# Performance work log

Hardware: AMD Instinct MI355X
Metric: run time of the kernel (lower is better)

Reference implementation:

```python
import jax, jax.numpy as jnp
import numpy as np

B, T, D, H, STRIDE, MLP = 2, 2048, 1024, 16, 8, 4096
HD = D // H
EPS = 1e-5


def _ln(x, g, b):
    m = x.mean(-1, keepdims=True)
    v = x.var(-1, keepdims=True)
    return (x - m) * jax.lax.rsqrt(v + EPS) * g + b


def setup_inputs() -> dict:
    key = jax.random.key(0)
    ks = jax.random.split(key, 6)
    s = lambda k, shape: (jax.random.normal(k, shape, jnp.float32) * 0.02)
    return {
        "x": jax.random.normal(ks[0], (B, T, D), jnp.float32),
        "w_in": s(ks[1], (3 * D, D)),   # torch in_proj_weight
        "b_in": jnp.zeros((3 * D,), jnp.float32),
        "w_out": s(ks[2], (D, D)),      # attn out_proj
        "b_out": jnp.zeros((D,), jnp.float32),
        "w1": s(ks[3], (MLP, D)),       # mlp first Linear (torch layout [out,in])
        "b1": jnp.zeros((MLP,), jnp.float32),
        "w2": s(ks[4], (D, MLP)),       # mlp second Linear
        "b2": jnp.zeros((D,), jnp.float32),
        "ln1_g": jnp.ones((D,), jnp.float32),
        "ln1_b": jnp.zeros((D,), jnp.float32),
        "ln2_g": jnp.ones((D,), jnp.float32),
        "ln2_b": jnp.zeros((D,), jnp.float32),
    }


def reference(x, w_in, b_in, w_out, b_out, w1, b1, w2, b2,
              ln1_g, ln1_b, ln2_g, ln2_b):
    Bs, Ts, Ds = x.shape
    xn = _ln(x, ln1_g, ln1_b)
    # fused qkv projection (torch Linear: y = x @ W.T + b)
    qkv = xn @ w_in.T + b_in                              # [B,T,3D]
    q, k, v = jnp.split(qkv, 3, axis=-1)
    to_heads = lambda t: t.reshape(Bs, Ts, H, HD).transpose(0, 2, 1, 3)
    q, k, v = to_heads(q), to_heads(k), to_heads(v)       # [B,H,T,hd]
    scores = jnp.einsum("bhqd,bhkd->bhqk", q, k) / jnp.sqrt(jnp.float32(HD))
    # mask: rows at multiples of STRIDE attend everywhere; others only to self
    idx = jnp.arange(Ts)
    allowed = ((idx % STRIDE) == 0)[:, None] | (idx[:, None] == idx[None, :])
    scores = jnp.where(allowed, scores, -jnp.inf)
    attn = jax.nn.softmax(scores, axis=-1)
    o = jnp.einsum("bhqk,bhkd->bhqd", attn, v)            # [B,H,T,hd]
    o = o.transpose(0, 2, 1, 3).reshape(Bs, Ts, Ds)
    o = o @ w_out.T + b_out
    x = x + o
    xn = _ln(x, ln2_g, ln2_b)
    h = jax.nn.gelu(xn @ w1.T + b1, approximate=False)    # torch nn.GELU default = exact
    x = x + (h @ w2.T + b2)
    return x
```

## Files before the change

### kernel.cpp

```cpp
#include <hip/hip_runtime.h>

#define D_ 1024
#define T_ 2048
#define B_ 2
#define H_ 16
#define MLP_ 4096
#define NTOK (B_*T_)
#define QG 256
#define L2E 1.44269504088896340736f

typedef float f32x4 __attribute__((ext_vector_type(4)));
typedef __bf16 bf16x8 __attribute__((ext_vector_type(8)));

__device__ __forceinline__ unsigned short f2bf(float f) {
  unsigned int u = __float_as_uint(f);
  u += 0x7fff + ((u >> 16) & 1);
  return (unsigned short)(u >> 16);
}

__device__ __forceinline__ float wave_sum(float v) {
  for (int o = 32; o > 0; o >>= 1) v += __shfl_down(v, o, 64);
  return v;
}

__device__ __forceinline__ void gload16(const unsigned short* g, unsigned short* l) {
  __builtin_amdgcn_global_load_lds(
      (const __attribute__((address_space(1))) void*)g,
      (__attribute__((address_space(3))) void*)l, 16, 0, 0);
}

#define N4_WIN  786432
#define N4_WOUT 262144
#define N4_W1   1048576
#define N4_W2   1048576
__global__ void cast_all_kernel(const float* __restrict__ w_in,
                                const float* __restrict__ w_out,
                                const float* __restrict__ w1,
                                const float* __restrict__ w2,
                                unsigned short* __restrict__ o_in,
                                unsigned short* __restrict__ o_out,
                                unsigned short* __restrict__ o1,
                                unsigned short* __restrict__ o2) {
  int i = blockIdx.x * 256 + threadIdx.x;
  const float* src; unsigned short* dst; int j = i;
  if (i < N4_WIN) { src = w_in; dst = o_in; }
  else if ((j -= N4_WIN) < N4_WOUT) { src = w_out; dst = o_out; }
  else if ((j -= N4_WOUT) < N4_W1) { src = w1; dst = o1; }
  else { j -= N4_W1; src = w2; dst = o2; }
  float4 v = ((const float4*)src)[j];
  ushort4 o;
  o.x = f2bf(v.x); o.y = f2bf(v.y); o.z = f2bf(v.z); o.w = f2bf(v.w);
  ((ushort4*)dst)[j] = o;
}

__global__ void ln_kernel(const float* __restrict__ x, const float* __restrict__ g,
                          const float* __restrict__ b, unsigned short* __restrict__ out) {
  int row = blockIdx.x;
  int tid = threadIdx.x;
  int wave = tid >> 6, lane = tid & 63;
  float4 v = ((const float4*)(x + (size_t)row * D_))[tid];
  float s  = v.x + v.y + v.z + v.w;
  float s2 = v.x*v.x + v.y*v.y + v.z*v.z + v.w*v.w;
  s = wave_sum(s); s2 = wave_sum(s2);
  __shared__ float r1[4], r2[4];
  if (lane == 0) { r1[wave] = s; r2[wave] = s2; }
  __syncthreads();
  float ts  = r1[0] + r1[1] + r1[2] + r1[3];
  float ts2 = r2[0] + r2[1] + r2[2] + r2[3];
  float mean = ts * (1.0f / D_);
  float var  = ts2 * (1.0f / D_) - mean * mean;
  float rs = rsqrtf(var + 1e-5f);
  float4 gv = ((const float4*)g)[tid];
  float4 bv = ((const float4*)b)[tid];
  ushort4 o;
  o.x = f2bf((v.x - mean) * rs * gv.x + bv.x);
  o.y = f2bf((v.y - mean) * rs * gv.y + bv.y);
  o.z = f2bf((v.z - mean) * rs * gv.z + bv.z);
  o.w = f2bf((v.w - mean) * rs * gv.w + bv.w);
  ((ushort4*)(out + (size_t)row * D_))[tid] = o;
}

__global__ void reduce_ln_kernel(const float* __restrict__ part,
                                 const float* __restrict__ x,
                                 const float* __restrict__ bias,
                                 const float* __restrict__ g,
                                 const float* __restrict__ b,
                                 float* __restrict__ x1,
                                 unsigned short* __restrict__ xn2) {
  int row = blockIdx.x;
  int tid = threadIdx.x;
  int wave = tid >> 6, lane = tid & 63;
  size_t base = (size_t)row * (D_ / 4) + tid;
  float4 v = ((const float4*)x)[base];
  float4 bo = ((const float4*)bias)[tid];
  v.x += bo.x; v.y += bo.y; v.z += bo.z; v.w += bo.w;
#pragma unroll
  for (int c = 0; c < 2; ++c) {
    float4 p = ((const float4*)part)[(size_t)c * (NTOK * (D_ / 4)) + base];
    v.x += p.x; v.y += p.y; v.z += p.z; v.w += p.w;
  }
  ((float4*)x1)[base] = v;
  float s  = v.x + v.y + v.z + v.w;
  float s2 = v.x*v.x + v.y*v.y + v.z*v.z + v.w*v.w;
  s = wave_sum(s); s2 = wave_sum(s2);
  __shared__ float r1[4], r2[4];
  if (lane == 0) { r1[wave] = s; r2[wave] = s2; }
  __syncthreads();
  float ts  = r1[0] + r1[1] + r1[2] + r1[3];
  float ts2 = r2[0] + r2[1] + r2[2] + r2[3];
  float mean = ts * (1.0f / D_);
  float var  = ts2 * (1.0f / D_) - mean * mean;
  float rs = rsqrtf(var + 1e-5f);
  float4 gv = ((const float4*)g)[tid];
  float4 bv = ((const float4*)b)[tid];
  ushort4 o;
  o.x = f2bf((v.x - mean) * rs * gv.x + bv.x);
  o.y = f2bf((v.y - mean) * rs * gv.y + bv.y);
  o.z = f2bf((v.z - mean) * rs * gv.z + bv.z);
  o.w = f2bf((v.w - mean) * rs * gv.w + bv.w);
  ((ushort4*)xn2)[base] = o;
}

__global__ void reduce_out_kernel(const float* __restrict__ part,
                                  const float* __restrict__ x1,
                                  const float* __restrict__ bias,
                                  float* __restrict__ out) {
  int i = blockIdx.x * 256 + threadIdx.x;
  float4 v = ((const float4*)x1)[i];
  float4 bo = ((const float4*)bias)[i & (D_ / 4 - 1)];
  v.x += bo.x; v.y += bo.y; v.z += bo.z; v.w += bo.w;
#pragma unroll
  for (int c = 0; c < 4; ++c) {
    float4 p = ((const float4*)part)[(size_t)c * (NTOK * (D_ / 4)) + i];
    v.x += p.x; v.y += p.y; v.z += p.z; v.w += p.w;
  }
  ((float4*)out)[i] = v;
}

template<int EPI, int SWIZ, int LDA, int LDB, int LDC>
__global__ __launch_bounds__(256)
void gemm_kernel(const unsigned short* __restrict__ A, size_t sA,
                 const unsigned short* __restrict__ Bm, size_t sB,
                 void* __restrict__ Cv, size_t sC,
                 const float* __restrict__ bias,
                 unsigned short* __restrict__ aux1,
                 unsigned short* __restrict__ aux2,
                 int K, int nx, int ny, int kshift) {
  __shared__ __align__(16) unsigned short As[128 * 64];
  __shared__ __align__(16) unsigned short Bs[128 * 64];
  const int flat = blockIdx.x;
  int bx, by;
  if (SWIZ == 1) {
    bx = flat / ny; by = flat - bx * ny;
  } else {
    const int sxc = nx >> 1;
    const int nSuper = sxc * (ny >> 2);
    int s = flat % nSuper, pos = flat / nSuper;
    int sx = s % sxc, sy = s / sxc;
    bx = sx * 2 + (pos & 1);
    by = sy * 4 + (pos >> 1);
  }
  const int bz = blockIdx.z;
  const int batch = bz >> kshift;
  const int kOff  = (bz & ((1 << kshift) - 1)) * K;
  const int m0 = by * 128;
  const int n0 = bx * 128;
  const int tid = threadIdx.x;
  const int lane = tid & 63, wave = tid >> 6;
  const int wm = (wave >> 1) * 64, wn = (wave & 1) * 64;
  const int fr = lane & 15, q = lane >> 4;
  const int f0 = ((q)     ^ (fr & 7)) << 3;
  const int f1 = ((4 + q) ^ (fr & 7)) << 3;

  const unsigned short* aP[4];
  const unsigned short* bP[4];
  unsigned short* dA[4];
  unsigned short* dB[4];
#pragma unroll
  for (int p = 0; p < 4; ++p) {
    int l = p * 256 + tid;
    int r = l >> 3;
    int cg = (l & 7) ^ (r & 7);
    aP[p] = A  + (size_t)batch * sA + kOff + (size_t)(m0 + r) * LDA + cg * 8;
    bP[p] = Bm + (size_t)batch * sB + kOff + (size_t)(n0 + r) * LDB + cg * 8;
    dA[p] = &As[l * 8];
    dB[p] = &Bs[l * 8];
  }

  f32x4 acc[4][4] = {};
  for (int ko = 0; ko < K; ko += 64) {
    __syncthreads();
#pragma unroll
    for (int p = 0; p < 4; ++p) {
      gload16(aP[p], dA[p]); gload16(bP[p], dB[p]);
      aP[p] += 64; bP[p] += 64;
    }
    __syncthreads();
    {
      bf16x8 af[4], bfr[4];
#pragma unroll
      for (int i = 0; i < 4; ++i) af[i]  = *(const bf16x8*)&As[(wm + i * 16 + fr) * 64 + f0];
#pragma unroll
      for (int j = 0; j < 4; ++j) bfr[j] = *(const bf16x8*)&Bs[(wn + j * 16 + fr) * 64 + f0];
#pragma unroll
      for (int i = 0; i < 4; ++i)
#pragma unroll
        for (int j = 0; j < 4; ++j)
          acc[i][j] = __builtin_amdgcn_mfma_f32_16x16x32_bf16(af[i], bfr[j], acc[i][j], 0, 0, 0);
    }
    {
      bf16x8 af[4], bfr[4];
#pragma unroll
      for (int i = 0; i < 4; ++i) af[i]  = *(const bf16x8*)&As[(wm + i * 16 + fr) * 64 + f1];
#pragma unroll
      for (int j = 0; j < 4; ++j) bfr[j] = *(const bf16x8*)&Bs[(wn + j * 16 + fr) * 64 + f1];
#pragma unroll
      for (int i = 0; i < 4; ++i)
#pragma unroll
        for (int j = 0; j < 4; ++j)
          acc[i][j] = __builtin_amdgcn_mfma_f32_16x16x32_bf16(af[i], bfr[j], acc[i][j], 0, 0, 0);
    }
  }

  const int col = lane & 15, rbase = (lane >> 4) * 4;
#pragma unroll
  for (int i = 0; i < 4; ++i) {
#pragma unroll
    for (int j = 0; j < 4; ++j) {
      int gn = n0 + wn + j * 16 + col;
      int gmb = m0 + wm + i * 16 + rbase;
      float bv = (EPI == 2 || EPI == 8) ? bias[gn] : 0.0f;
#pragma unroll
      for (int r = 0; r < 4; ++r) {
        int gm = gmb + r;
        float v = acc[i][j][r] + bv;
        if (EPI == 2) {
          float u = v * (1.5957691216f + 0.0713548162f * v * v);
          float gl = v / (1.0f + exp2f(-L2E * u));
          ((unsigned short*)Cv)[(size_t)gm * LDC + gn] = f2bf(gl);
        } else if (EPI == 7) {
          ((float*)Cv)[(size_t)bz * sC + (size_t)gm * LDC + gn] = v;
        } else if (EPI == 8) {
          int sec = gn >> 10;
          int hh = (gn >> 6) & (H_ - 1);
          int dd = gn & 63;
          int t = gm & (T_ - 1);
          int b = gm >> 11;
          unsigned short bf = f2bf(v);
          if (sec == 0) {
            if (!(t & 7))
              aux1[(((size_t)(b * H_ + hh)) * QG + (t >> 3)) * 64 + dd] = bf;
          } else if (sec == 1) {
            aux2[(((size_t)(b * H_ + hh)) * T_ + t) * 64 + dd] = bf;
          } else {
            ((unsigned short*)Cv)[(size_t)gm * D_ + (gn - 2 * D_)] = bf;
          }
        }
      }
    }
  }
}

template<int EPI>
__global__ __launch_bounds__(512)
void gemm256_kernel(const unsigned short* __restrict__ A, int LDA,
                    const unsigned short* __restrict__ Bm, int LDB,
                    void* __restrict__ Cv, size_t sC, int LDC,
                    const float* __restrict__ bias, int K, int nxs) {
  __shared__ __align__(16) unsigned short As[2 * 16384];
  __shared__ __align__(16) unsigned short Bs[2 * 16384];
  const int tid = threadIdx.x;
  const int lane = tid & 63, w = tid >> 6;
  const int wm = w >> 2, wn = w & 3;
  const int fr = lane & 15, q = lane >> 4, xr = fr & 7;

  const int nwg = gridDim.x;
  const int bid = blockIdx.x;
  const int l = (bid & 7) * (nwg >> 3) + (bid >> 3);
  const int bx = l & ((1 << nxs) - 1), by = l >> nxs;
  const int m0 = by * 256, n0 = bx * 256;
  const int kOff = blockIdx.z * K;

  const unsigned short* aS[4];
  const unsigned short* bS[4];
#pragma unroll
  for (int s = 0; s < 4; ++s) {
    int ls = s * 512 + tid;
    int r = ls >> 3;
    int cg = (ls & 7) ^ (r & 7);
    aS[s] = A  + (size_t)(m0 + r) * LDA + kOff + cg * 8;
    bS[s] = Bm + (size_t)(n0 + r) * LDB + kOff + cg * 8;
  }
  const int NT = K >> 6;

#pragma unroll
  for (int s = 0; s < 4; ++s) {
    gload16(aS[s], &As[s * 4096 + tid * 8]);
    gload16(bS[s], &Bs[s * 4096 + tid * 8]);
  }
#pragma unroll
  for (int s = 0; s < 4; ++s) {
    gload16(aS[s] + 64, &As[16384 + s * 4096 + tid * 8]);
    gload16(bS[s] + 64, &Bs[16384 + s * 4096 + tid * 8]);
  }
  asm volatile("s_waitcnt vmcnt(8)");
  __builtin_amdgcn_sched_barrier(0);
  __builtin_amdgcn_s_barrier();
  __builtin_amdgcn_sched_barrier(0);

  const int aOff = ((wm * 128 + fr) << 7) + ((q ^ xr) << 4);
  const int bOff = ((wn * 64 + fr) << 7) + ((q ^ xr) << 4);

  f32x4 acc[8][4] = {};

  for (int t = 0; t < NT; ++t) {
    const int cb = (t & 1) << 15;
    const char* Ab = (const char*)As + cb;
    const char* Bb = (const char*)Bs + cb;
    unsigned short* Ad = (unsigned short*)((char*)As + cb);
    unsigned short* Bd = (unsigned short*)((char*)Bs + cb);
    const int ko2 = (t + 2) << 6;
    bf16x8 af[2][4], bfr[2][4];

#pragma unroll
    for (int i = 0; i < 4; ++i) {
      af[0][i] = *(const bf16x8*)(Ab + aOff + i * 2048);
      af[1][i] = *(const bf16x8*)(Ab + (aOff ^ 64) + i * 2048);
    }
#pragma unroll
    for (int j = 0; j < 2; ++j) {
      bfr[0][j] = *(const bf16x8*)(Bb + bOff + j * 2048);
      bfr[1][j] = *(const bf16x8*)(Bb + (bOff ^ 64) + j * 2048);
    }
    __builtin_amdgcn_sched_barrier(0);
    __builtin_amdgcn_s_barrier();
    __builtin_amdgcn_sched_barrier(0);
    __builtin_amdgcn_s_setprio(1);
#pragma unroll
    for (int i = 0; i < 4; ++i)
#pragma unroll
      for (int j = 0; j < 2; ++j) {
        acc[i][j] = __builtin_amdgcn_mfma_f32_16x16x32_bf16(af[0][i], bfr[0][j], acc[i][j], 0, 0, 0);
        acc[i][j] = __builtin_amdgcn_mfma_f32_16x16x32_bf16(af[1][i], bfr[1][j], acc[i][j], 0, 0, 0);
      }
    __builtin_amdgcn_s_setprio(0);
    __builtin_amdgcn_sched_barrier(0);
    __builtin_amdgcn_s_barrier();
    __builtin_amdgcn_sched_barrier(0);

#pragma unroll
    for (int j = 2; j < 4; ++j) {
      bfr[0][j] = *(const bf16x8*)(Bb + bOff + j * 2048);
      bfr[1][j] = *(const bf16x8*)(Bb + (bOff ^ 64) + j * 2048);
    }
    if (t + 2 < NT) {
      gload16(aS[0] + ko2, Ad + tid * 8);
      gload16(aS[2] + ko2, Ad + 2 * 4096 + tid * 8);
    }
    __builtin_amdgcn_sched_barrier(0);
    __builtin_amdgcn_s_barrier();
    __builtin_amdgcn_sched_barrier(0);
    __builtin_amdgcn_s_setprio(1);
#pragma unroll
    for (int i = 0; i < 4; ++i)
#pragma unroll
      for (int j = 0; j < 2; ++j) {
        acc[i][2 + j] = __builtin_amdgcn_mfma_f32_16x16x32_bf16(af[0][i], bfr[0][2 + j], acc[i][2 + j], 0, 0, 0);
        acc[i][2 + j] = __builtin_amdgcn_mfma_f32_16x16x32_bf16(af[1][i], bfr[1][2 + j], acc[i][2 + j], 0, 0, 0);
      }
    __builtin_amdgcn_s_setprio(0);
    __builtin_amdgcn_sched_barrier(0);
    __builtin_amdgcn_s_barrier();
    __builtin_amdgcn_sched_barrier(0);

#pragma unroll
    for (int i = 0; i < 4; ++i) {
      af[0][i] = *(const bf16x8*)(Ab + (aOff + 8192) + i * 2048);
      af[1][i] = *(const bf16x8*)(Ab + ((aOff + 8192) ^ 64) + i * 2048);
    }
    if (t + 2 < NT) {
      gload16(bS[0] + ko2, Bd + tid * 8);
      gload16(bS[1] + ko2, Bd + 4096 + tid * 8);
      gload16(bS[2] + ko2, Bd + 2 * 4096 + tid * 8);
      gload16(bS[3] + ko2, Bd + 3 * 4096 + tid * 8);
    }
    __builtin_amdgcn_sched_barrier(0);
    __builtin_amdgcn_s_barrier();
    __builtin_amdgcn_sched_barrier(0);
    __builtin_amdgcn_s_setprio(1);
#pragma unroll
    for (int i = 0; i < 4; ++i)
#pragma unroll
      for (int j = 0; j < 2; ++j) {
        acc[4 + i][j] = __builtin_amdgcn_mfma_f32_16x16x32_bf16(af[0][i], bfr[0][j], acc[4 + i][j], 0, 0, 0);
        acc[4 + i][j] = __builtin_amdgcn_mfma_f32_16x16x32_bf16(af[1][i], bfr[1][j], acc[4 + i][j], 0, 0, 0);
      }
    __builtin_amdgcn_s_setprio(0);
    __builtin_amdgcn_sched_barrier(0);
    __builtin_amdgcn_s_barrier();
    __builtin_amdgcn_sched_barrier(0);

    if (t + 2 < NT) {
      gload16(aS[1] + ko2, Ad + 4096 + tid * 8);
      gload16(aS[3] + ko2, Ad + 3 * 4096 + tid * 8);
    }
    if (t + 1 < NT) {
      if (t + 2 < NT) asm volatile("s_waitcnt vmcnt(8)");
      else            asm volatile("s_waitcnt vmcnt(0)");
    }
    __builtin_amdgcn_sched_barrier(0);
    __builtin_amdgcn_s_barrier();
    __builtin_amdgcn_sched_barrier(0);
    __builtin_amdgcn_s_setprio(1);
#pragma unroll
    for (int i = 0; i < 4; ++i)
#pragma unroll
      for (int j = 0; j < 2; ++j) {
        acc[4 + i][2 + j] = __builtin_amdgcn_mfma_f32_16x16x32_bf16(af[0][i], bfr[0][2 + j], acc[4 + i][2 + j], 0, 0, 0);
        acc[4 + i][2 + j] = __builtin_amdgcn_mfma_f32_16x16x32_bf16(af[1][i], bfr[1][2 + j], acc[4 + i][2 + j], 0, 0, 0);
      }
    __builtin_amdgcn_s_setprio(0);
    __builtin_amdgcn_sched_barrier(0);
    __builtin_amdgcn_s_barrier();
    __builtin_amdgcn_sched_barrier(0);
  }

  const int col = lane & 15, rbase = (lane >> 4) * 4;
  const int gm0 = m0 + wm * 128 + rbase;
  const int gn0 = n0 + wn * 64 + col;
#pragma unroll
  for (int mi = 0; mi < 8; ++mi) {
#pragma unroll
    for (int j = 0; j < 4; ++j) {
      int gn = gn0 + j * 16;
      float bv = (EPI == 2) ? bias[gn] : 0.0f;
#pragma unroll
      for (int r = 0; r < 4; ++r) {
        int gm = gm0 + mi * 16 + r;
        float v = acc[mi][j][r] + bv;
        if (EPI == 2) {
          float u = v * (1.5957691216f + 0.0713548162f * v * v);
          float gl = v / (1.0f + exp2f(-L2E * u));
          ((unsigned short*)Cv)[(size_t)gm * LDC + gn] = f2bf(gl);
        } else {
          ((float*)Cv)[(size_t)blockIdx.z * sC + (size_t)gm * LDC + gn] = v;
        }
      }
    }
  }
}

__global__ void vtrans_kernel(const unsigned short* __restrict__ vcomp,
                              unsigned short* __restrict__ Vt) {
  int blk = blockIdx.x;
  int tchunk = blk & 31;
  int bh = blk >> 5;
  int h = bh & (H_ - 1), b = bh >> 4;
  int t0 = tchunk * 64;
  __shared__ unsigned short ls[64][66];
  int tid = threadIdx.x;
#pragma unroll
  for (int it = 0; it < 16; ++it) {
    int linear = it * 256 + tid;
    int d = linear & 63, tl = linear >> 6;
    ls[d][tl] = vcomp[((size_t)(b * T_ + t0 + tl)) * D_ + h * 64 + d];
  }
  __syncthreads();
#pragma unroll
  for (int it = 0; it < 16; ++it) {
    int linear = it * 256 + tid;
    int tl = linear & 63, d = linear >> 6;
    Vt[((size_t)(bh * 64 + d)) * T_ + t0 + tl] = ls[d][tl];
  }
}

__global__ __launch_bounds__(256)
void flash_kernel(const unsigned short* __restrict__ Qg,
                  const unsigned short* __restrict__ Kh,
                  const unsigned short* __restrict__ Vt,
                  float* __restrict__ Opart,
                  float* __restrict__ ml) {
  const int kc = blockIdx.x, qt = blockIdx.y, bh = blockIdx.z;
  const int tid = threadIdx.x;
  const int lane = tid & 63, w = tid >> 6;
  const int fr = lane & 15, quad = lane >> 4;

  __shared__ __align__(16) unsigned short Qs[64 * 64];
  __shared__ __align__(16) unsigned short Ks[128 * 64];
  __shared__ __align__(16) unsigned short Vs[64 * 128];
  __shared__ __align__(16) unsigned short Ps[4 * 16 * 128];

  const unsigned short* Qbase = Qg + ((size_t)bh * 256 + qt * 64) * 64;
#pragma unroll
  for (int p = 0; p < 2; ++p) {
    int linear = p * 256 + tid;
    int r = linear >> 3, c = linear & 7;
    gload16(Qbase + r * 64 + (c ^ (r & 7)) * 8, &Qs[linear * 8]);
  }

  float m_run[4], l_run[4];
  f32x4 O[4] = {};
#pragma unroll
  for (int r = 0; r < 4; ++r) { m_run[r] = -3.0e38f; l_run[r] = 0.f; }

  const unsigned short* Kc = Kh + ((size_t)bh * T_ + kc * 512) * 64;
  const unsigned short* Vc = Vt + (size_t)bh * 64 * T_ + kc * 512;
  unsigned short* Pw = &Ps[w * 2048];
  const int arow = w * 16 + fr;

  for (int kt = 0; kt < 4; ++kt) {
    __syncthreads();
#pragma unroll
    for (int p = 0; p < 4; ++p) {
      int linear = p * 256 + tid;
      int r = linear >> 3, c = linear & 7;
      gload16(Kc + (size_t)(kt * 128 + r) * 64 + (c ^ (r & 7)) * 8, &Ks[linear * 8]);
    }
#pragma unroll
    for (int p = 0; p < 4; ++p) {
      int linear = p * 256 + tid;
      int r = linear >> 4, c = linear & 15;
      gload16(Vc + (size_t)r * T_ + kt * 128 + (c ^ (r & 7)) * 8, &Vs[linear * 8]);
    }
    __syncthreads();

    f32x4 s[8] = {};
    bf16x8 aq[2];
#pragma unroll
    for (int ks = 0; ks < 2; ++ks)
      aq[ks] = *(const bf16x8*)&Qs[arow * 64 + ((ks * 4 + quad) ^ (fr & 7)) * 8];
#pragma unroll
    for (int nf = 0; nf < 8; ++nf) {
      int krow = nf * 16 + fr;
#pragma unroll
      for (int ks = 0; ks < 2; ++ks) {
        bf16x8 bk = *(const bf16x8*)&Ks[krow * 64 + ((ks * 4 + quad) ^ (fr & 7)) * 8];
        s[nf] = __builtin_amdgcn_mfma_f32_16x16x32_bf16(aq[ks], bk, s[nf], 0, 0, 0);
      }
    }
    float alpha[4], rowsum[4];
#pragma unroll
    for (int r = 0; r < 4; ++r) {
      float mt = -3.0e38f;
#pragma unroll
      for (int nf = 0; nf < 8; ++nf) { s[nf][r] *= 0.125f; mt = fmaxf(mt, s[nf][r]); }
#pragma unroll
      for (int x = 1; x < 16; x <<= 1) mt = fmaxf(mt, __shfl_xor(mt, x, 64));
      float mn = fmaxf(m_run[r], mt);
      alpha[r] = exp2f((m_run[r] - mn) * L2E);
      m_run[r] = mn;
      rowsum[r] = 0.f;
    }
#pragma unroll
    for (int nf = 0; nf < 8; ++nf)
#pragma unroll
      for (int r = 0; r < 4; ++r) {
        float p = exp2f((s[nf][r] - m_run[r]) * L2E);
        s[nf][r] = p; rowsum[r] += p;
      }
#pragma unroll
    for (int r = 0; r < 4; ++r) {
#pragma unroll
      for (int x = 1; x < 16; x <<= 1) rowsum[r] += __shfl_xor(rowsum[r], x, 64);
      l_run[r] = l_run[r] * alpha[r] + rowsum[r];
    }
#pragma unroll
    for (int nf = 0; nf < 8; ++nf)
#pragma unroll
      for (int r = 0; r < 4; ++r) {
        int m = quad * 4 + r;
        int c = nf * 2 + (fr >> 3);
        Pw[m * 128 + ((c ^ (m & 7)) * 8) + (fr & 7)] = f2bf(s[nf][r]);
      }
#pragma unroll
    for (int nf2 = 0; nf2 < 4; ++nf2)
#pragma unroll
      for (int r = 0; r < 4; ++r) O[nf2][r] *= alpha[r];
#pragma unroll
    for (int ks2 = 0; ks2 < 4; ++ks2) {
      bf16x8 ap = *(const bf16x8*)&Pw[fr * 128 + (((ks2 * 4 + quad) ^ (fr & 7)) * 8)];
#pragma unroll
      for (int nf2 = 0; nf2 < 4; ++nf2) {
        int vrow = nf2 * 16 + fr;
        bf16x8 bv = *(const bf16x8*)&Vs[vrow * 128 + (((ks2 * 4 + quad) ^ (fr & 7)) * 8)];
        O[nf2] = __builtin_amdgcn_mfma_f32_16x16x32_bf16(ap, bv, O[nf2], 0, 0, 0);
      }
    }
  }

  int qbase = qt * 64 + w * 16;
  float* Ob = Opart + (((size_t)bh * 4 + kc) * 256 + qbase) * 64;
#pragma unroll
  for (int nf2 = 0; nf2 < 4; ++nf2)
#pragma unroll
    for (int r = 0; r < 4; ++r)
      Ob[(size_t)(quad * 4 + r) * 64 + nf2 * 16 + fr] = O[nf2][r];
  if (fr == 0) {
#pragma unroll
    for (int r = 0; r < 4; ++r) {
      size_t mi = ((((size_t)bh * 4 + kc) * 256) + qbase + quad * 4 + r) * 2;
      ml[mi] = m_run[r]; ml[mi + 1] = l_run[r];
    }
  }
}

__global__ void combine_kernel(const float* __restrict__ Opart,
                               const float* __restrict__ ml,
                               unsigned short* __restrict__ vcomp) {
  int idx = blockIdx.x * 256 + threadIdx.x;
  int c = idx & (D_ - 1);
  int qi = (idx >> 10) & (QG - 1);
  int b = idx >> 18;
  int h = c >> 6, d = c & 63;
  int bh = b * H_ + h;
  float m[4], l[4];
  float M = -3.0e38f;
#pragma unroll
  for (int ch = 0; ch < 4; ++ch) {
    size_t r = ((size_t)bh * 4 + ch) * 256 + qi;
    m[ch] = ml[r * 2]; l[ch] = ml[r * 2 + 1];
    M = fmaxf(M, m[ch]);
  }
  float osum = 0.f, lsum = 0.f;
#pragma unroll
  for (int ch = 0; ch < 4; ++ch) {
    size_t r = ((size_t)bh * 4 + ch) * 256 + qi;
    float wgt = exp2f((m[ch] - M) * L2E);
    osum += wgt * Opart[r * 64 + d];
    lsum += wgt * l[ch];
  }
  vcomp[((size_t)(b * T_ + qi * 8)) * D_ + c] = f2bf(osum / lsum);
}

extern "C" void kernel_launch(void* const* d_in, const int* in_sizes, int n_in,
                              void* d_out, int out_size, void* d_ws, size_t ws_size,
                              hipStream_t stream) {
  const float* x     = (const float*)d_in[0];
  const float* w_in  = (const float*)d_in[1];
  const float* b_in  = (const float*)d_in[2];
  const float* w_out = (const float*)d_in[3];
  const float* b_out = (const float*)d_in[4];
  const float* w1    = (const float*)d_in[5];
  const float* b1    = (const float*)d_in[6];
  const float* w2    = (const float*)d_in[7];
  const float* b2    = (const float*)d_in[8];
  const float* ln1_g = (const float*)d_in[9];
  const float* ln1_b = (const float*)d_in[10];
  const float* ln2_g = (const float*)d_in[11];
  const float* ln2_b = (const float*)d_in[12];
  float* out = (float*)d_out;

  char* ws = (char*)d_ws;
  size_t off = 0;
  auto alloc = [&](size_t bytes) -> void* {
    void* p = ws + off;
    off += (bytes + 255) & ~(size_t)255;
    return p;
  };
  unsigned short* w_inb = (unsigned short*)alloc((size_t)3 * D_ * D_ * 2);
  unsigned short* w_outb= (unsigned short*)alloc((size_t)D_ * D_ * 2);
  unsigned short* w1b   = (unsigned short*)alloc((size_t)MLP_ * D_ * 2);
  unsigned short* w2b   = (unsigned short*)alloc((size_t)D_ * MLP_ * 2);
  unsigned short* vcomp = (unsigned short*)alloc((size_t)NTOK * D_ * 2);
  float*          x1    = (float*)         alloc((size_t)NTOK * D_ * 4);
  unsigned short* xn2   = (unsigned short*)alloc((size_t)NTOK * D_ * 2);
  unsigned short* h     = (unsigned short*)alloc((size_t)NTOK * MLP_ * 2);
  char* U = (char*)alloc((size_t)4 * NTOK * D_ * 4);
  float*          P2    = (float*)U;
  unsigned short* xn    = (unsigned short*)U;
  unsigned short* Qg    = (unsigned short*)(U + 8388608);
  unsigned short* Kh    = (unsigned short*)(U + 12582912);
  unsigned short* Vt    = (unsigned short*)(U + 20971520);
  float*          Opart = (float*)         (U + 29360128);
  float*          mlbuf = (float*)         (U + 37748736);

  cast_all_kernel<<<(N4_WIN + N4_WOUT + N4_W1 + N4_W2) / 256, 256, 0, stream>>>(
      w_in, w_out, w1, w2, w_inb, w_outb, w1b, w2b);

  ln_kernel<<<NTOK, 256, 0, stream>>>(x, ln1_g, ln1_b, xn);

  gemm_kernel<8, 2, D_, D_, 3 * D_><<<dim3(24 * 32, 1, 1), 256, 0, stream>>>(
      xn, 0, w_inb, 0, vcomp, 0, b_in, Qg, Kh, D_, 24, 32, 0);

  vtrans_kernel<<<1024, 256, 0, stream>>>(vcomp, Vt);

  flash_kernel<<<dim3(4, 4, 32), 256, 0, stream>>>(Qg, Kh, Vt, Opart, mlbuf);

  combine_kernel<<<2048, 256, 0, stream>>>(Opart, mlbuf, vcomp);

  gemm_kernel<7, 1, D_, D_, D_><<<dim3(8 * 32, 1, 2), 256, 0, stream>>>(
      vcomp, 0, w_outb, 0, P2, (size_t)NTOK * D_, nullptr, nullptr, nullptr,
      512, 8, 32, 1);

  reduce_ln_kernel<<<NTOK, 256, 0, stream>>>(P2, x, b_out, ln2_g, ln2_b, x1, xn2);

  gemm256_kernel<2><<<dim3(256, 1, 1), 512, 0, stream>>>(
      xn2, D_, w1b, D_, h, 0, MLP_, b1, D_, 4);

  gemm256_kernel<7><<<dim3(64, 1, 4), 512, 0, stream>>>(
      h, MLP_, w2b, MLP_, P2, (size_t)NTOK * D_, D_, nullptr, 1024, 2);

  reduce_out_kernel<<<4096, 256, 0, stream>>>(P2, x1, b2, out);
}
```

Baseline: 332.5 us.

## Drop split-K partial buffers and fuse bias/residual into GEMM epilogues

The out-projection and MLP-down GEMMs no longer use split-K with fp32 partial buffers and separate reduce kernels. A 128x128 GEMM now writes bias plus residual directly, and LayerNorm2 runs as a plain ln_kernel on x1. The QKV projection moves to the pipelined 256x256 kernel, whose epilogue scatters into the head layouts. This removes the partial-buffer traffic and two reduction launches, but the down-projection (K=4096) now runs on only 256 blocks with no split-K, which lowers parallelism for long K.

```diff
diff --git a/kernel.cpp b/kernel.cpp
--- a/kernel.cpp
+++ b/kernel.cpp
@@ -80,89 +80,23 @@
   ((ushort4*)(out + (size_t)row * D_))[tid] = o;
 }
 
-__global__ void reduce_ln_kernel(const float* __restrict__ part,
-                                 const float* __restrict__ x,
-                                 const float* __restrict__ bias,
-                                 const float* __restrict__ g,
-                                 const float* __restrict__ b,
-                                 float* __restrict__ x1,
-                                 unsigned short* __restrict__ xn2) {
-  int row = blockIdx.x;
-  int tid = threadIdx.x;
-  int wave = tid >> 6, lane = tid & 63;
-  size_t base = (size_t)row * (D_ / 4) + tid;
-  float4 v = ((const float4*)x)[base];
-  float4 bo = ((const float4*)bias)[tid];
-  v.x += bo.x; v.y += bo.y; v.z += bo.z; v.w += bo.w;
-#pragma unroll
-  for (int c = 0; c < 2; ++c) {
-    float4 p = ((const float4*)part)[(size_t)c * (NTOK * (D_ / 4)) + base];
-    v.x += p.x; v.y += p.y; v.z += p.z; v.w += p.w;
-  }
-  ((float4*)x1)[base] = v;
-  float s  = v.x + v.y + v.z + v.w;
-  float s2 = v.x*v.x + v.y*v.y + v.z*v.z + v.w*v.w;
-  s = wave_sum(s); s2 = wave_sum(s2);
-  __shared__ float r1[4], r2[4];
-  if (lane == 0) { r1[wave] = s; r2[wave] = s2; }
-  __syncthreads();
-  float ts  = r1[0] + r1[1] + r1[2] + r1[3];
-  float ts2 = r2[0] + r2[1] + r2[2] + r2[3];
-  float mean = ts * (1.0f / D_);
-  float var  = ts2 * (1.0f / D_) - mean * mean;
-  float rs = rsqrtf(var + 1e-5f);
-  float4 gv = ((const float4*)g)[tid];
-  float4 bv = ((const float4*)b)[tid];
-  ushort4 o;
-  o.x = f2bf((v.x - mean) * rs * gv.x + bv.x);
-  o.y = f2bf((v.y - mean) * rs * gv.y + bv.y);
-  o.z = f2bf((v.z - mean) * rs * gv.z + bv.z);
-  o.w = f2bf((v.w - mean) * rs * gv.w + bv.w);
-  ((ushort4*)xn2)[base] = o;
-}
-
-__global__ void reduce_out_kernel(const float* __restrict__ part,
-                                  const float* __restrict__ x1,
-                                  const float* __restrict__ bias,
-                                  float* __restrict__ out) {
-  int i = blockIdx.x * 256 + threadIdx.x;
-  float4 v = ((const float4*)x1)[i];
-  float4 bo = ((const float4*)bias)[i & (D_ / 4 - 1)];
-  v.x += bo.x; v.y += bo.y; v.z += bo.z; v.w += bo.w;
-#pragma unroll
-  for (int c = 0; c < 4; ++c) {
-    float4 p = ((const float4*)part)[(size_t)c * (NTOK * (D_ / 4)) + i];
-    v.x += p.x; v.y += p.y; v.z += p.z; v.w += p.w;
-  }
-  ((float4*)out)[i] = v;
-}
-
-template<int EPI, int SWIZ, int LDA, int LDB, int LDC>
+template<int LDA, int LDB>
 __global__ __launch_bounds__(256)
-void gemm_kernel(const unsigned short* __restrict__ A, size_t sA,
-                 const unsigned short* __restrict__ Bm, size_t sB,
-                 void* __restrict__ Cv, size_t sC,
-                 const float* __restrict__ bias,
-                 unsigned short* __restrict__ aux1,
-                 unsigned short* __restrict__ aux2,
-                 int K, int nx, int ny, int kshift) {
+void gemm128_kernel(const unsigned short* __restrict__ A,
+                    const unsigned short* __restrict__ Bm,
+                    float* __restrict__ Cv,
+                    const float* __restrict__ bias,
+                    const float* __restrict__ xres,
+                    int K, int nx, int ny) {
   __shared__ __align__(16) unsigned short As[128 * 64];
   __shared__ __align__(16) unsigned short Bs[128 * 64];
   const int flat = blockIdx.x;
-  int bx, by;
-  if (SWIZ == 1) {
-    bx = flat / ny; by = flat - bx * ny;
-  } else {
-    const int sxc = nx >> 1;
-    const int nSuper = sxc * (ny >> 2);
-    int s = flat % nSuper, pos = flat / nSuper;
-    int sx = s % sxc, sy = s / sxc;
-    bx = sx * 2 + (pos & 1);
-    by = sy * 4 + (pos >> 1);
-  }
-  const int bz = blockIdx.z;
-  const int batch = bz >> kshift;
-  const int kOff  = (bz & ((1 << kshift) - 1)) * K;
+  const int sxc = nx >> 1;
+  const int nSuper = sxc * (ny >> 2);
+  int s = flat % nSuper, pos = flat / nSuper;
+  int sx = s % sxc, sy = s / sxc;
+  int bx = sx * 2 + (pos & 1);
+  int by = sy * 4 + (pos >> 1);
   const int m0 = by * 128;
   const int n0 = bx * 128;
   const int tid = threadIdx.x;
@@ -181,8 +115,8 @@
     int l = p * 256 + tid;
     int r = l >> 3;
     int cg = (l & 7) ^ (r & 7);
-    aP[p] = A  + (size_t)batch * sA + kOff + (size_t)(m0 + r) * LDA + cg * 8;
-    bP[p] = Bm + (size_t)batch * sB + kOff + (size_t)(n0 + r) * LDB + cg * 8;
+    aP[p] = A  + (size_t)(m0 + r) * LDA + cg * 8;
+    bP[p] = Bm + (size_t)(n0 + r) * LDB + cg * 8;
     dA[p] = &As[l * 8];
     dB[p] = &Bs[l * 8];
   }
@@ -229,18 +163,185 @@
     for (int j = 0; j < 4; ++j) {
       int gn = n0 + wn + j * 16 + col;
       int gmb = m0 + wm + i * 16 + rbase;
-      float bv = (EPI == 2 || EPI == 8) ? bias[gn] : 0.0f;
+      float bv = bias[gn];
 #pragma unroll
       for (int r = 0; r < 4; ++r) {
         int gm = gmb + r;
-        float v = acc[i][j][r] + bv;
+        size_t idx = (size_t)gm * D_ + gn;
+        Cv[idx] = acc[i][j][r] + bv + xres[idx];
+      }
+    }
+  }
+}
+
+template<int EPI>
+__global__ __launch_bounds__(512)
+void gemm256_kernel(const unsigned short* __restrict__ A, int LDA,
+                    const unsigned short* __restrict__ Bm, int LDB,
+                    void* __restrict__ Cv, size_t sC, int LDC,
+                    const float* __restrict__ bias,
+                    unsigned short* __restrict__ aux1,
+                    unsigned short* __restrict__ aux2,
+                    int K, int nx) {
+  __shared__ __align__(16) unsigned short As[2 * 16384];
+  __shared__ __align__(16) unsigned short Bs[2 * 16384];
+  const int tid = threadIdx.x;
+  const int lane = tid & 63, w = tid >> 6;
+  const int wm = w >> 2, wn = w & 3;
+  const int fr = lane & 15, q = lane >> 4, xr = fr & 7;
+
+  const int nwg = gridDim.x;
+  const int bid = blockIdx.x;
+  const int l = (bid & 7) * (nwg >> 3) + (bid >> 3);
+  const int bx = l % nx, by = l / nx;
+  const int m0 = by * 256, n0 = bx * 256;
+
+  const unsigned short* aS[4];
+  const unsigned short* bS[4];
+#pragma unroll
+  for (int s = 0; s < 4; ++s) {
+    int ls = s * 512 + tid;
+    int r = ls >> 3;
+    int cg = (ls & 7) ^ (r & 7);
+    aS[s] = A  + (size_t)(m0 + r) * LDA + cg * 8;
+    bS[s] = Bm + (size_t)(n0 + r) * LDB + cg * 8;
+  }
+  const int NT = K >> 6;
+
+#pragma unroll
+  for (int s = 0; s < 4; ++s) {
+    gload16(aS[s], &As[s * 4096 + tid * 8]);
+    gload16(bS[s], &Bs[s * 4096 + tid * 8]);
+  }
+#pragma unroll
+  for (int s = 0; s < 4; ++s) {
+    gload16(aS[s] + 64, &As[16384 + s * 4096 + tid * 8]);
+    gload16(bS[s] + 64, &Bs[16384 + s * 4096 + tid * 8]);
+  }
+  asm volatile("s_waitcnt vmcnt(8)");
+  __builtin_amdgcn_sched_barrier(0);
+  __builtin_amdgcn_s_barrier();
+
+  const int aOff = ((wm * 128 + fr) << 7) + ((q ^ xr) << 4);
+  const int bOff = ((wn * 64 + fr) << 7) + ((q ^ xr) << 4);
+
+  f32x4 acc[8][4] = {};
+
+  for (int t = 0; t < NT; ++t) {
+    const int cb = (t & 1) << 15;
+    const char* Ab = (const char*)As + cb;
+    const char* Bb = (const char*)Bs + cb;
+    unsigned short* Ad = (unsigned short*)((char*)As + cb);
+    unsigned short* Bd = (unsigned short*)((char*)Bs + cb);
+    const int ko2 = (t + 2) << 6;
+    bf16x8 af[2][4], bfr[2][4];
+
+#pragma unroll
+    for (int i = 0; i < 4; ++i) {
+      af[0][i] = *(const bf16x8*)(Ab + aOff + i * 2048);
+      af[1][i] = *(const bf16x8*)(Ab + (aOff ^ 64) + i * 2048);
+    }
+#pragma unroll
+    for (int j = 0; j < 2; ++j) {
+      bfr[0][j] = *(const bf16x8*)(Bb + bOff + j * 2048);
+      bfr[1][j] = *(const bf16x8*)(Bb + (bOff ^ 64) + j * 2048);
+    }
+    __builtin_amdgcn_s_barrier();
+    __builtin_amdgcn_s_setprio(1);
+#pragma unroll
+    for (int i = 0; i < 4; ++i)
+#pragma unroll
+      for (int j = 0; j < 2; ++j) {
+        acc[i][j] = __builtin_amdgcn_mfma_f32_16x16x32_bf16(af[0][i], bfr[0][j], acc[i][j], 0, 0, 0);
+        acc[i][j] = __builtin_amdgcn_mfma_f32_16x16x32_bf16(af[1][i], bfr[1][j], acc[i][j], 0, 0, 0);
+      }
+    __builtin_amdgcn_s_setprio(0);
+    __builtin_amdgcn_s_barrier();
+
+#pragma unroll
+    for (int j = 2; j < 4; ++j) {
+      bfr[0][j] = *(const bf16x8*)(Bb + bOff + j * 2048);
+      bfr[1][j] = *(const bf16x8*)(Bb + (bOff ^ 64) + j * 2048);
+    }
+    if (t + 2 < NT) {
+      gload16(aS[0] + ko2, Ad + tid * 8);
+      gload16(aS[2] + ko2, Ad + 2 * 4096 + tid * 8);
+    }
+    __builtin_amdgcn_s_barrier();
+    __builtin_amdgcn_s_setprio(1);
+#pragma unroll
+    for (int i = 0; i < 4; ++i)
+#pragma unroll
+      for (int j = 0; j < 2; ++j) {
+        acc[i][2 + j] = __builtin_amdgcn_mfma_f32_16x16x32_bf16(af[0][i], bfr[0][2 + j], acc[i][2 + j], 0, 0, 0);
+        acc[i][2 + j] = __builtin_amdgcn_mfma_f32_16x16x32_bf16(af[1][i], bfr[1][2 + j], acc[i][2 + j], 0, 0, 0);
+      }
+    __builtin_amdgcn_s_setprio(0);
+    __builtin_amdgcn_s_barrier();
+
+#pragma unroll
+    for (int i = 0; i < 4; ++i) {
+      af[0][i] = *(const bf16x8*)(Ab + (aOff + 8192) + i * 2048);
+      af[1][i] = *(const bf16x8*)(Ab + ((aOff + 8192) ^ 64) + i * 2048);
+    }
+    if (t + 2 < NT) {
+      gload16(bS[0] + ko2, Bd + tid * 8);
+      gload16(bS[1] + ko2, Bd + 4096 + tid * 8);
+      gload16(bS[2] + ko2, Bd + 2 * 4096 + tid * 8);
+      gload16(bS[3] + ko2, Bd + 3 * 4096 + tid * 8);
+    }
+    __builtin_amdgcn_s_barrier();
+    __builtin_amdgcn_s_setprio(1);
+#pragma unroll
+    for (int i = 0; i < 4; ++i)
+#pragma unroll
+      for (int j = 0; j < 2; ++j) {
+        acc[4 + i][j] = __builtin_amdgcn_mfma_f32_16x16x32_bf16(af[0][i], bfr[0][j], acc[4 + i][j], 0, 0, 0);
+        acc[4 + i][j] = __builtin_amdgcn_mfma_f32_16x16x32_bf16(af[1][i], bfr[1][j], acc[4 + i][j], 0, 0, 0);
+      }
+    __builtin_amdgcn_s_setprio(0);
+    __builtin_amdgcn_s_barrier();
+
+    if (t + 2 < NT) {
+      gload16(aS[1] + ko2, Ad + 4096 + tid * 8);
+      gload16(aS[3] + ko2, Ad + 3 * 4096 + tid * 8);
+    }
+    if (t + 1 < NT) {
+      if (t + 2 < NT) asm volatile("s_waitcnt vmcnt(8)");
+      else            asm volatile("s_waitcnt vmcnt(0)");
+      __builtin_amdgcn_sched_barrier(0);
+    }
+    __builtin_amdgcn_s_barrier();
+    __builtin_amdgcn_s_setprio(1);
+#pragma unroll
+    for (int i = 0; i < 4; ++i)
+#pragma unroll
+      for (int j = 0; j < 2; ++j) {
+        acc[4 + i][2 + j] = __builtin_amdgcn_mfma_f32_16x16x32_bf16(af[0][i], bfr[0][2 + j], acc[4 + i][2 + j], 0, 0, 0);
+        acc[4 + i][2 + j] = __builtin_amdgcn_mfma_f32_16x16x32_bf16(af[1][i], bfr[1][2 + j], acc[4 + i][2 + j], 0, 0, 0);
+      }
+    __builtin_amdgcn_s_setprio(0);
+    __builtin_amdgcn_s_barrier();
+  }
+
+  const int col = lane & 15, rbase = (lane >> 4) * 4;
+  const int gm0 = m0 + wm * 128 + rbase;
+  const int gn0 = n0 + wn * 64 + col;
+#pragma unroll
+  for (int mi = 0; mi < 8; ++mi) {
+#pragma unroll
+    for (int j = 0; j < 4; ++j) {
+      int gn = gn0 + j * 16;
+      float bv = bias[gn];
+#pragma unroll
+      for (int r = 0; r < 4; ++r) {
+        int gm = gm0 + mi * 16 + r;
+        float v = acc[mi][j][r] + bv;
         if (EPI == 2) {
           float u = v * (1.5957691216f + 0.0713548162f * v * v);
           float gl = v / (1.0f + exp2f(-L2E * u));
           ((unsigned short*)Cv)[(size_t)gm * LDC + gn] = f2bf(gl);
-        } else if (EPI == 7) {
-          ((float*)Cv)[(size_t)bz * sC + (size_t)gm * LDC + gn] = v;
-        } else if (EPI == 8) {
+        } else {
           int sec = gn >> 10;
           int hh = (gn >> 6) & (H_ - 1);
           int dd = gn & 63;
@@ -255,195 +356,6 @@
           } else {
             ((unsigned short*)Cv)[(size_t)gm * D_ + (gn - 2 * D_)] = bf;
           }
-        }
-      }
-    }
-  }
-}
-
-template<int EPI>
-__global__ __launch_bounds__(512)
-void gemm256_kernel(const unsigned short* __restrict__ A, int LDA,
-                    const unsigned short* __restrict__ Bm, int LDB,
-                    void* __restrict__ Cv, size_t sC, int LDC,
-                    const float* __restrict__ bias, int K, int nxs) {
-  __shared__ __align__(16) unsigned short As[2 * 16384];
-  __shared__ __align__(16) unsigned short Bs[2 * 16384];
-  const int tid = threadIdx.x;
-  const int lane = tid & 63, w = tid >> 6;
-  const int wm = w >> 2, wn = w & 3;
-  const int fr = lane & 15, q = lane >> 4, xr = fr & 7;
-
-  const int nwg = gridDim.x;
-  const int bid = blockIdx.x;
-  const int l = (bid & 7) * (nwg >> 3) + (bid >> 3);
-  const int bx = l & ((1 << nxs) - 1), by = l >> nxs;
-  const int m0 = by * 256, n0 = bx * 256;
-  const int kOff = blockIdx.z * K;
-
-  const unsigned short* aS[4];
-  const unsigned short* bS[4];
-#pragma unroll
-  for (int s = 0; s < 4; ++s) {
-    int ls = s * 512 + tid;
-    int r = ls >> 3;
-    int cg = (ls & 7) ^ (r & 7);
-    aS[s] = A  + (size_t)(m0 + r) * LDA + kOff + cg * 8;
-    bS[s] = Bm + (size_t)(n0 + r) * LDB + kOff + cg * 8;
-  }
-  const int NT = K >> 6;
-
-#pragma unroll
-  for (int s = 0; s < 4; ++s) {
-    gload16(aS[s], &As[s * 4096 + tid * 8]);
-    gload16(bS[s], &Bs[s * 4096 + tid * 8]);
-  }
-#pragma unroll
-  for (int s = 0; s < 4; ++s) {
-    gload16(aS[s] + 64, &As[16384 + s * 4096 + tid * 8]);
-    gload16(bS[s] + 64, &Bs[16384 + s * 4096 + tid * 8]);
-  }
-  asm volatile("s_waitcnt vmcnt(8)");
-  __builtin_amdgcn_sched_barrier(0);
-  __builtin_amdgcn_s_barrier();
-  __builtin_amdgcn_sched_barrier(0);
-
-  const int aOff = ((wm * 128 + fr) << 7) + ((q ^ xr) << 4);
-  const int bOff = ((wn * 64 + fr) << 7) + ((q ^ xr) << 4);
-
-  f32x4 acc[8][4] = {};
-
-  for (int t = 0; t < NT; ++t) {
-    const int cb = (t & 1) << 15;
-    const char* Ab = (const char*)As + cb;
-    const char* Bb = (const char*)Bs + cb;
-    unsigned short* Ad = (unsigned short*)((char*)As + cb);
-    unsigned short* Bd = (unsigned short*)((char*)Bs + cb);
-    const int ko2 = (t + 2) << 6;
-    bf16x8 af[2][4], bfr[2][4];
-
-#pragma unroll
-    for (int i = 0; i < 4; ++i) {
-      af[0][i] = *(const bf16x8*)(Ab + aOff + i * 2048);
-      af[1][i] = *(const bf16x8*)(Ab + (aOff ^ 64) + i * 2048);
-    }
-#pragma unroll
-    for (int j = 0; j < 2; ++j) {
-      bfr[0][j] = *(const bf16x8*)(Bb + bOff + j * 2048);
-      bfr[1][j] = *(const bf16x8*)(Bb + (bOff ^ 64) + j * 2048);
-    }
-    __builtin_amdgcn_sched_barrier(0);
-    __builtin_amdgcn_s_barrier();
-    __builtin_amdgcn_sched_barrier(0);
-    __builtin_amdgcn_s_setprio(1);
-#pragma unroll
-    for (int i = 0; i < 4; ++i)
-#pragma unroll
-      for (int j = 0; j < 2; ++j) {
-        acc[i][j] = __builtin_amdgcn_mfma_f32_16x16x32_bf16(af[0][i], bfr[0][j], acc[i][j], 0, 0, 0);
-        acc[i][j] = __builtin_amdgcn_mfma_f32_16x16x32_bf16(af[1][i], bfr[1][j], acc[i][j], 0, 0, 0);
-      }
-    __builtin_amdgcn_s_setprio(0);
-    __builtin_amdgcn_sched_barrier(0);
-    __builtin_amdgcn_s_barrier();
-    __builtin_amdgcn_sched_barrier(0);
-
-#pragma unroll
-    for (int j = 2; j < 4; ++j) {
-      bfr[0][j] = *(const bf16x8*)(Bb + bOff + j * 2048);
-      bfr[1][j] = *(const bf16x8*)(Bb + (bOff ^ 64) + j * 2048);
-    }
-    if (t + 2 < NT) {
-      gload16(aS[0] + ko2, Ad + tid * 8);
-      gload16(aS[2] + ko2, Ad + 2 * 4096 + tid * 8);
-    }
-    __builtin_amdgcn_sched_barrier(0);
-    __builtin_amdgcn_s_barrier();
-    __builtin_amdgcn_sched_barrier(0);
-    __builtin_amdgcn_s_setprio(1);
-#pragma unroll
-    for (int i = 0; i < 4; ++i)
-#pragma unroll
-      for (int j = 0; j < 2; ++j) {
-        acc[i][2 + j] = __builtin_amdgcn_mfma_f32_16x16x32_bf16(af[0][i], bfr[0][2 + j], acc[i][2 + j], 0, 0, 0);
-        acc[i][2 + j] = __builtin_amdgcn_mfma_f32_16x16x32_bf16(af[1][i], bfr[1][2 + j], acc[i][2 + j], 0, 0, 0);
-      }
-    __builtin_amdgcn_s_setprio(0);
-    __builtin_amdgcn_sched_barrier(0);
-    __builtin_amdgcn_s_barrier();
-    __builtin_amdgcn_sched_barrier(0);
-
-#pragma unroll
-    for (int i = 0; i < 4; ++i) {
-      af[0][i] = *(const bf16x8*)(Ab + (aOff + 8192) + i * 2048);
-      af[1][i] = *(const bf16x8*)(Ab + ((aOff + 8192) ^ 64) + i * 2048);
-    }
-    if (t + 2 < NT) {
-      gload16(bS[0] + ko2, Bd + tid * 8);
-      gload16(bS[1] + ko2, Bd + 4096 + tid * 8);
-      gload16(bS[2] + ko2, Bd + 2 * 4096 + tid * 8);
-      gload16(bS[3] + ko2, Bd + 3 * 4096 + tid * 8);
-    }
-    __builtin_amdgcn_sched_barrier(0);
-    __builtin_amdgcn_s_barrier();
-    __builtin_amdgcn_sched_barrier(0);
-    __builtin_amdgcn_s_setprio(1);
-#pragma unroll
-    for (int i = 0; i < 4; ++i)
-#pragma unroll
-      for (int j = 0; j < 2; ++j) {
-        acc[4 + i][j] = __builtin_amdgcn_mfma_f32_16x16x32_bf16(af[0][i], bfr[0][j], acc[4 + i][j], 0, 0, 0);
-        acc[4 + i][j] = __builtin_amdgcn_mfma_f32_16x16x32_bf16(af[1][i], bfr[1][j], acc[4 + i][j], 0, 0, 0);
-      }
-    __builtin_amdgcn_s_setprio(0);
-    __builtin_amdgcn_sched_barrier(0);
-    __builtin_amdgcn_s_barrier();
-    __builtin_amdgcn_sched_barrier(0);
-
-    if (t + 2 < NT) {
-      gload16(aS[1] + ko2, Ad + 4096 + tid * 8);
-      gload16(aS[3] + ko2, Ad + 3 * 4096 + tid * 8);
-    }
-    if (t + 1 < NT) {
-      if (t + 2 < NT) asm volatile("s_waitcnt vmcnt(8)");
-      else            asm volatile("s_waitcnt vmcnt(0)");
-    }
-    __builtin_amdgcn_sched_barrier(0);
-    __builtin_amdgcn_s_barrier();
-    __builtin_amdgcn_sched_barrier(0);
-    __builtin_amdgcn_s_setprio(1);
-#pragma unroll
-    for (int i = 0; i < 4; ++i)
-#pragma unroll
-      for (int j = 0; j < 2; ++j) {
-        acc[4 + i][2 + j] = __builtin_amdgcn_mfma_f32_16x16x32_bf16(af[0][i], bfr[0][2 + j], acc[4 + i][2 + j], 0, 0, 0);
-        acc[4 + i][2 + j] = __builtin_amdgcn_mfma_f32_16x16x32_bf16(af[1][i], bfr[1][2 + j], acc[4 + i][2 + j], 0, 0, 0);
-      }
-    __builtin_amdgcn_s_setprio(0);
-    __builtin_amdgcn_sched_barrier(0);
-    __builtin_amdgcn_s_barrier();
-    __builtin_amdgcn_sched_barrier(0);
-  }
-
-  const int col = lane & 15, rbase = (lane >> 4) * 4;
-  const int gm0 = m0 + wm * 128 + rbase;
-  const int gn0 = n0 + wn * 64 + col;
-#pragma unroll
-  for (int mi = 0; mi < 8; ++mi) {
-#pragma unroll
-    for (int j = 0; j < 4; ++j) {
-      int gn = gn0 + j * 16;
-      float bv = (EPI == 2) ? bias[gn] : 0.0f;
-#pragma unroll
-      for (int r = 0; r < 4; ++r) {
-        int gm = gm0 + mi * 16 + r;
-        float v = acc[mi][j][r] + bv;
-        if (EPI == 2) {
-          float u = v * (1.5957691216f + 0.0713548162f * v * v);
-          float gl = v / (1.0f + exp2f(-L2E * u));
-          ((unsigned short*)Cv)[(size_t)gm * LDC + gn] = f2bf(gl);
-        } else {
-          ((float*)Cv)[(size_t)blockIdx.z * sC + (size_t)gm * LDC + gn] = v;
         }
       }
     }
@@ -665,8 +577,7 @@
   float*          x1    = (float*)         alloc((size_t)NTOK * D_ * 4);
   unsigned short* xn2   = (unsigned short*)alloc((size_t)NTOK * D_ * 2);
   unsigned short* h     = (unsigned short*)alloc((size_t)NTOK * MLP_ * 2);
-  char* U = (char*)alloc((size_t)4 * NTOK * D_ * 4);
-  float*          P2    = (float*)U;
+  char* U = (char*)alloc((size_t)40 * 1024 * 1024);
   unsigned short* xn    = (unsigned short*)U;
   unsigned short* Qg    = (unsigned short*)(U + 8388608);
   unsigned short* Kh    = (unsigned short*)(U + 12582912);
@@ -679,8 +590,8 @@
 
   ln_kernel<<<NTOK, 256, 0, stream>>>(x, ln1_g, ln1_b, xn);
 
-  gemm_kernel<8, 2, D_, D_, 3 * D_><<<dim3(24 * 32, 1, 1), 256, 0, stream>>>(
-      xn, 0, w_inb, 0, vcomp, 0, b_in, Qg, Kh, D_, 24, 32, 0);
+  gemm256_kernel<8><<<dim3(192, 1, 1), 512, 0, stream>>>(
+      xn, D_, w_inb, D_, vcomp, 0, 3 * D_, b_in, Qg, Kh, D_, 12);
 
   vtrans_kernel<<<1024, 256, 0, stream>>>(vcomp, Vt);
 
@@ -688,17 +599,14 @@
 
   combine_kernel<<<2048, 256, 0, stream>>>(Opart, mlbuf, vcomp);
 
-  gemm_kernel<7, 1, D_, D_, D_><<<dim3(8 * 32, 1, 2), 256, 0, stream>>>(
-      vcomp, 0, w_outb, 0, P2, (size_t)NTOK * D_, nullptr, nullptr, nullptr,
-      512, 8, 32, 1);
-
-  reduce_ln_kernel<<<NTOK, 256, 0, stream>>>(P2, x, b_out, ln2_g, ln2_b, x1, xn2);
+  gemm128_kernel<D_, D_><<<256, 256, 0, stream>>>(
+      vcomp, w_outb, x1, b_out, x, D_, 8, 32);
+
+  ln_kernel<<<NTOK, 256, 0, stream>>>(x1, ln2_g, ln2_b, xn2);
 
   gemm256_kernel<2><<<dim3(256, 1, 1), 512, 0, stream>>>(
-      xn2, D_, w1b, D_, h, 0, MLP_, b1, D_, 4);
-
-  gemm256_kernel<7><<<dim3(64, 1, 4), 512, 0, stream>>>(
-      h, MLP_, w2b, MLP_, P2, (size_t)NTOK * D_, D_, nullptr, 1024, 2);
-
-  reduce_out_kernel<<<4096, 256, 0, stream>>>(P2, x1, b2, out);
-}
+      xn2, D_, w1b, D_, h, 0, MLP_, b1, nullptr, nullptr, D_, 16);
+
+  gemm128_kernel<MLP_, MLP_><<<256, 256, 0, stream>>>(
+      h, w2b, out, b2, x1, MLP_, 8, 32);
+}
```

Measured after the change: 346.2 us. 1.04x slower.
